# Kernel tuning notes

Measured on AMD Instinct MI355X. Metric: run time of the kernel, lower is better.

The kernel has to match this reference:

```python
import jax, jax.numpy as jnp
import numpy as np


def setup_inputs() -> dict:
    key = jax.random.key(0)
    k1, k2, k3 = jax.random.split(key, 3)
    B, H, S, D = 2, 16, 2048, 64
    q = jax.random.normal(k1, (B, H, S, D), dtype=jnp.float32)
    k = jax.random.normal(k2, (B, H, S, D), dtype=jnp.float32)
    v = jax.random.normal(k3, (B, H, S, D), dtype=jnp.float32)
    return {"q": q, "k": k, "v": v}


def reference(q, k, v):
    # q,k,v: [B,H,S,D]; causal attention with 1/sqrt(D) scaling, fp32 softmax.
    scale = 1.0 / (q.shape[-1] ** 0.5)
    scores = jnp.einsum('bhqd,bhkd->bhqk', q * scale, k)  # [B,H,S,S]
    S = scores.shape[-1]
    causal_mask = jnp.triu(jnp.ones((S, S), dtype=bool), k=1)
    scores = jnp.where(causal_mask, -jnp.inf, scores)
    attn = jax.nn.softmax(scores.astype(jnp.float32), axis=-1).astype(q.dtype)
    output = jnp.einsum('bhqk,bhkd->bhqd', attn, v)
    # Module also returns an all-zeros attn_weights placeholder of shape [B,H,S,S]
    attn_weights = jnp.zeros(scores.shape, dtype=q.dtype)
    return (output, attn_weights)
```

## Files before the change

### kernel.cpp

```cpp
#include <hip/hip_runtime.h>


typedef __bf16 bf16x8 __attribute__((ext_vector_type(8)));
typedef float f32x4 __attribute__((ext_vector_type(4)));

#define LOG2E 1.44269504088896340736f

__device__ __forceinline__ unsigned short f2bf(float f) {
  unsigned int u = __float_as_uint(f);
  u += 0x7fffu + ((u >> 16) & 1u);
  return (unsigned short)(u >> 16);
}

constexpr int Sdim = 2048, Ddim = 64, BHn = 32;
constexpr int STiles = 16;
constexpr int LDK = 72;
constexpr int OUT0 = BHn * Sdim * Ddim;
constexpr size_t FILL_PER_BH = 1048576;

__device__ __forceinline__ int vswz_m(int d) { return ((d >> 2) ^ (d >> 5)) & 7; }

__global__ __launch_bounds__(256, 2)
void flash_causal_kernel(const float* __restrict__ Q, const float* __restrict__ K,
                         const float* __restrict__ V, float* __restrict__ out) {
  __shared__ unsigned short Klds[2][64 * LDK];
  __shared__ unsigned short Vlds[2][64 * LDK];
  __shared__ unsigned short Plds[4][2][16 * LDK];

  const int tid  = threadIdx.x;
  const int wave = tid >> 6;
  const int lane = tid & 63;
  const int quad = lane >> 4;
  const int l15  = lane & 15;

  const int bh = blockIdx.x & (BHn - 1);
  const int g  = (int)(blockIdx.x >> 5);
  const int s  = (g & 1) ? (STiles - 1) - (g >> 1) : (g >> 1);
  const int jmax = 2 * s + 1;

  const int base  = bh * Sdim * Ddim;
  const int qbase = s * 128;

  bf16x8 aq[2][2];
  #pragma unroll
  for (int f = 0; f < 2; ++f) {
    const float* qp = Q + base + (qbase + 64 * f + wave * 16 + l15) * Ddim + quad * 8;
    #pragma unroll
    for (int s2 = 0; s2 < 2; ++s2) {
      float4 a = *(const float4*)(qp + 32 * s2);
      float4 b = *(const float4*)(qp + 32 * s2 + 4);
      union { unsigned short u[8]; bf16x8 v; } u;
      u.u[0] = f2bf(a.x * 0.125f); u.u[1] = f2bf(a.y * 0.125f);
      u.u[2] = f2bf(a.z * 0.125f); u.u[3] = f2bf(a.w * 0.125f);
      u.u[4] = f2bf(b.x * 0.125f); u.u[5] = f2bf(b.y * 0.125f);
      u.u[6] = f2bf(b.z * 0.125f); u.u[7] = f2bf(b.w * 0.125f);
      aq[f][s2] = u.v;
    }
  }

  f32x4 ot[2][4];
  #pragma unroll
  for (int f = 0; f < 2; ++f)
    #pragma unroll
    for (int t = 0; t < 4; ++t) ot[f][t] = (f32x4){0.f, 0.f, 0.f, 0.f};
  float mrun[2] = {-__builtin_inff(), -__builtin_inff()};
  float lrun[2] = {0.f, 0.f};

  const float4* kg4 = (const float4*)(K + base);
  const float4* vg4 = (const float4*)(V + base);
  float4 kf[4], vf[4];

  auto ldtile = [&](int j) {
    const float4* kp = kg4 + j * 1024;
    const float4* vp = vg4 + j * 1024;
    #pragma unroll
    for (int i = 0; i < 4; ++i) { kf[i] = kp[i * 256 + tid]; vf[i] = vp[i * 256 + tid]; }
  };
  auto stage = [&](int buf) {
    #pragma unroll
    for (int i = 0; i < 4; ++i) {
      int lin = i * 256 + tid;
      int row = lin >> 4;
      int c4  = (lin & 15) << 2;
      uint2 t2;
      t2.x = (unsigned int)f2bf(kf[i].x) | ((unsigned int)f2bf(kf[i].y) << 16);
      t2.y = (unsigned int)f2bf(kf[i].z) | ((unsigned int)f2bf(kf[i].w) << 16);
      *(uint2*)&Klds[buf][row * LDK + c4] = t2;
      const int sw = vswz_m(c4) << 3;
      Vlds[buf][(c4 + 0) * LDK + (row ^ sw)] = f2bf(vf[i].x);
      Vlds[buf][(c4 + 1) * LDK + (row ^ sw)] = f2bf(vf[i].y);
      Vlds[buf][(c4 + 2) * LDK + (row ^ sw)] = f2bf(vf[i].z);
      Vlds[buf][(c4 + 3) * LDK + (row ^ sw)] = f2bf(vf[i].w);
    }
  };

  ldtile(0); stage(0); ldtile(1);

  for (int j = 0; j <= jmax; ++j) {
    __syncthreads();
    if (j < jmax) stage((j + 1) & 1);
    if (j + 2 <= jmax) ldtile(j + 2);

    const unsigned short* Kb = Klds[j & 1];
    const unsigned short* Vb = Vlds[j & 1];
    const bool f0act = (j <= 2 * s);

    f32x4 sc[2][4];
    #pragma unroll
    for (int f = 0; f < 2; ++f)
      #pragma unroll
      for (int t = 0; t < 4; ++t) sc[f][t] = (f32x4){0.f, 0.f, 0.f, 0.f};
    #pragma unroll
    for (int s2 = 0; s2 < 2; ++s2) {
      #pragma unroll
      for (int t = 0; t < 4; ++t) {
        bf16x8 ka = *(const bf16x8*)&Kb[(16 * t + l15) * LDK + 32 * s2 + quad * 8];
        sc[0][t] = __builtin_amdgcn_mfma_f32_16x16x32_bf16(ka, aq[0][s2], sc[0][t], 0, 0, 0);
        sc[1][t] = __builtin_amdgcn_mfma_f32_16x16x32_bf16(ka, aq[1][s2], sc[1][t], 0, 0, 0);
      }
    }

    #pragma unroll
    for (int f = 0; f < 2; ++f) {
      if (j == 2 * s + f) {
        const int qml = wave * 16 + l15;
        #pragma unroll
        for (int t = 0; t < 4; ++t)
          #pragma unroll
          for (int r = 0; r < 4; ++r)
            if (16 * t + 4 * quad + r > qml) sc[f][t][r] = -__builtin_inff();
      }
    }

    #pragma unroll
    for (int f = 0; f < 2; ++f) {
      if (f == 0 && !f0act) continue;
      float mx = sc[f][0][0];
      #pragma unroll
      for (int t = 0; t < 4; ++t)
        #pragma unroll
        for (int r = 0; r < 4; ++r) mx = fmaxf(mx, sc[f][t][r]);
      mx = fmaxf(mx, __shfl_xor(mx, 16));
      mx = fmaxf(mx, __shfl_xor(mx, 32));
      float mn    = fmaxf(mrun[f], mx);
      float alpha = __builtin_amdgcn_exp2f((mrun[f] - mn) * LOG2E);
      float msc   = mn * LOG2E;
      mrun[f] = mn;
      float rs = 0.f;
      #pragma unroll
      for (int t = 0; t < 4; ++t)
        #pragma unroll
        for (int r = 0; r < 4; ++r) {
          float p = __builtin_amdgcn_exp2f(fmaf(sc[f][t][r], LOG2E, -msc));
          sc[f][t][r] = p;
          rs += p;
        }
      rs += __shfl_xor(rs, 16);
      rs += __shfl_xor(rs, 32);
      lrun[f] = lrun[f] * alpha + rs;
      #pragma unroll
      for (int t = 0; t < 4; ++t)
        #pragma unroll
        for (int r = 0; r < 4; ++r) ot[f][t][r] *= alpha;
      #pragma unroll
      for (int t = 0; t < 4; ++t) {
        uint2 pw;
        pw.x = (unsigned int)f2bf(sc[f][t][0]) | ((unsigned int)f2bf(sc[f][t][1]) << 16);
        pw.y = (unsigned int)f2bf(sc[f][t][2]) | ((unsigned int)f2bf(sc[f][t][3]) << 16);
        *(uint2*)&Plds[wave][f][l15 * LDK + 16 * t + 4 * quad] = pw;
      }
    }

    #pragma unroll
    for (int s2 = 0; s2 < 2; ++s2) {
      bf16x8 pb0, pb1;
      if (f0act) pb0 = *(const bf16x8*)&Plds[wave][0][l15 * LDK + 32 * s2 + quad * 8];
      pb1 = *(const bf16x8*)&Plds[wave][1][l15 * LDK + 32 * s2 + quad * 8];
      #pragma unroll
      for (int t = 0; t < 4; ++t) {
        const int d = 16 * t + l15;
        bf16x8 va = *(const bf16x8*)&Vb[d * LDK + (((4 * s2 + quad) ^ vswz_m(d)) << 3)];
        if (f0act)
          ot[0][t] = __builtin_amdgcn_mfma_f32_16x16x32_bf16(va, pb0, ot[0][t], 0, 0, 0);
        ot[1][t] = __builtin_amdgcn_mfma_f32_16x16x32_bf16(va, pb1, ot[1][t], 0, 0, 0);
      }
    }
  }

  #pragma unroll
  for (int f = 0; f < 2; ++f) {
    float inv = 1.0f / lrun[f];
    float* orow = out + base + (qbase + 64 * f + wave * 16 + l15) * Ddim + 4 * quad;
    #pragma unroll
    for (int t = 0; t < 4; ++t) {
      f32x4 o4;
      o4.x = ot[f][t][0] * inv; o4.y = ot[f][t][1] * inv;
      o4.z = ot[f][t][2] * inv; o4.w = ot[f][t][3] * inv;
      *(f32x4*)(orow + 16 * t) = o4;
    }
  }

  {
    const int gp = (STiles - 1) - s;
    const int w  = 2 * gp + 1;
    const size_t start_f4 = (size_t)bh * FILL_PER_BH + (size_t)4096 * (gp * gp);
    const size_t count_f4 = (size_t)4096 * w;
    f32x4 z4 = (f32x4){0.f, 0.f, 0.f, 0.f};
    f32x4* zp = (f32x4*)(out + OUT0) + start_f4;
    for (size_t i = tid; i < count_f4; i += 256)
      __builtin_nontemporal_store(z4, zp + i);
  }
}

extern "C" void kernel_launch(void* const* d_in, const int* in_sizes, int n_in,
                              void* d_out, int out_size, void* d_ws, size_t ws_size,
                              hipStream_t stream) {
  const float* q = (const float*)d_in[0];
  const float* k = (const float*)d_in[1];
  const float* v = (const float*)d_in[2];
  float* out = (float*)d_out;
  dim3 grid(BHn * STiles);
  flash_causal_kernel<<<grid, dim3(256), 0, stream>>>(q, k, v, out);
}
```

Baseline: 586.6 us.

## Read K/V directly from global memory in fp16, drop LDS staging

Removes the double-buffered LDS staging of K and V and its barriers. Each wave now loads fp32 K and V straight from global memory (V with strided scalar loads) and converts them to fp16 using packed round-toward-zero conversions. MFMA switches from bf16 to f16, block scheduling becomes plain sequential in place of interleaved heavy/light tiles, and the zero fill is split evenly per block with ordinary stores in place of nontemporal ones. In exchange, each wave re-reads K and V from memory or cache, and the V loads are uncoalesced, so memory traffic and load latency per tile go up.

```diff
diff --git a/kernel.cpp b/kernel.cpp
--- a/kernel.cpp
+++ b/kernel.cpp
@@ -1,31 +1,31 @@
 #include <hip/hip_runtime.h>
 
 
-typedef __bf16 bf16x8 __attribute__((ext_vector_type(8)));
+typedef __fp16 f16x2 __attribute__((ext_vector_type(2)));
+typedef __fp16 f16x4 __attribute__((ext_vector_type(4)));
+typedef __fp16 f16x8 __attribute__((ext_vector_type(8)));
 typedef float f32x4 __attribute__((ext_vector_type(4)));
 
 #define LOG2E 1.44269504088896340736f
-
-__device__ __forceinline__ unsigned short f2bf(float f) {
-  unsigned int u = __float_as_uint(f);
-  u += 0x7fffu + ((u >> 16) & 1u);
-  return (unsigned short)(u >> 16);
-}
 
 constexpr int Sdim = 2048, Ddim = 64, BHn = 32;
 constexpr int STiles = 16;
 constexpr int LDK = 72;
 constexpr int OUT0 = BHn * Sdim * Ddim;
-constexpr size_t FILL_PER_BH = 1048576;
 
-__device__ __forceinline__ int vswz_m(int d) { return ((d >> 2) ^ (d >> 5)) & 7; }
+__device__ __forceinline__ f16x8 cvt8(float4 a, float4 b) {
+  union { f16x2 h2[4]; f16x8 v; } u;
+  u.h2[0] = __builtin_amdgcn_cvt_pkrtz(a.x, a.y);
+  u.h2[1] = __builtin_amdgcn_cvt_pkrtz(a.z, a.w);
+  u.h2[2] = __builtin_amdgcn_cvt_pkrtz(b.x, b.y);
+  u.h2[3] = __builtin_amdgcn_cvt_pkrtz(b.z, b.w);
+  return u.v;
+}
 
 __global__ __launch_bounds__(256, 2)
 void flash_causal_kernel(const float* __restrict__ Q, const float* __restrict__ K,
                          const float* __restrict__ V, float* __restrict__ out) {
-  __shared__ unsigned short Klds[2][64 * LDK];
-  __shared__ unsigned short Vlds[2][64 * LDK];
-  __shared__ unsigned short Plds[4][2][16 * LDK];
+  __shared__ __fp16 Plds[4][2][16 * LDK];
 
   const int tid  = threadIdx.x;
   const int wave = tid >> 6;
@@ -34,27 +34,25 @@
   const int l15  = lane & 15;
 
   const int bh = blockIdx.x & (BHn - 1);
-  const int g  = (int)(blockIdx.x >> 5);
-  const int s  = (g & 1) ? (STiles - 1) - (g >> 1) : (g >> 1);
+  const int s  = (int)(blockIdx.x >> 5);
   const int jmax = 2 * s + 1;
 
   const int base  = bh * Sdim * Ddim;
   const int qbase = s * 128;
 
-  bf16x8 aq[2][2];
+  f16x8 aq[2][2];
   #pragma unroll
   for (int f = 0; f < 2; ++f) {
-    const float* qp = Q + base + (qbase + 64 * f + wave * 16 + l15) * Ddim + quad * 8;
     #pragma unroll
     for (int s2 = 0; s2 < 2; ++s2) {
-      float4 a = *(const float4*)(qp + 32 * s2);
-      float4 b = *(const float4*)(qp + 32 * s2 + 4);
-      union { unsigned short u[8]; bf16x8 v; } u;
-      u.u[0] = f2bf(a.x * 0.125f); u.u[1] = f2bf(a.y * 0.125f);
-      u.u[2] = f2bf(a.z * 0.125f); u.u[3] = f2bf(a.w * 0.125f);
-      u.u[4] = f2bf(b.x * 0.125f); u.u[5] = f2bf(b.y * 0.125f);
-      u.u[6] = f2bf(b.z * 0.125f); u.u[7] = f2bf(b.w * 0.125f);
-      aq[f][s2] = u.v;
+      const float* qp = Q + base + (qbase + 64 * f + wave * 16 + l15) * Ddim
+                          + 32 * s2 + 8 * quad;
+      float4 a = *(const float4*)qp;
+      float4 b = *(const float4*)(qp + 4);
+      float4 as, bs;
+      as.x = a.x * 0.125f; as.y = a.y * 0.125f; as.z = a.z * 0.125f; as.w = a.w * 0.125f;
+      bs.x = b.x * 0.125f; bs.y = b.y * 0.125f; bs.z = b.z * 0.125f; bs.w = b.w * 0.125f;
+      aq[f][s2] = cvt8(as, bs);
     }
   }
 
@@ -66,43 +64,9 @@
   float mrun[2] = {-__builtin_inff(), -__builtin_inff()};
   float lrun[2] = {0.f, 0.f};
 
-  const float4* kg4 = (const float4*)(K + base);
-  const float4* vg4 = (const float4*)(V + base);
-  float4 kf[4], vf[4];
-
-  auto ldtile = [&](int j) {
-    const float4* kp = kg4 + j * 1024;
-    const float4* vp = vg4 + j * 1024;
-    #pragma unroll
-    for (int i = 0; i < 4; ++i) { kf[i] = kp[i * 256 + tid]; vf[i] = vp[i * 256 + tid]; }
-  };
-  auto stage = [&](int buf) {
-    #pragma unroll
-    for (int i = 0; i < 4; ++i) {
-      int lin = i * 256 + tid;
-      int row = lin >> 4;
-      int c4  = (lin & 15) << 2;
-      uint2 t2;
-      t2.x = (unsigned int)f2bf(kf[i].x) | ((unsigned int)f2bf(kf[i].y) << 16);
-      t2.y = (unsigned int)f2bf(kf[i].z) | ((unsigned int)f2bf(kf[i].w) << 16);
-      *(uint2*)&Klds[buf][row * LDK + c4] = t2;
-      const int sw = vswz_m(c4) << 3;
-      Vlds[buf][(c4 + 0) * LDK + (row ^ sw)] = f2bf(vf[i].x);
-      Vlds[buf][(c4 + 1) * LDK + (row ^ sw)] = f2bf(vf[i].y);
-      Vlds[buf][(c4 + 2) * LDK + (row ^ sw)] = f2bf(vf[i].z);
-      Vlds[buf][(c4 + 3) * LDK + (row ^ sw)] = f2bf(vf[i].w);
-    }
-  };
-
-  ldtile(0); stage(0); ldtile(1);
-
   for (int j = 0; j <= jmax; ++j) {
-    __syncthreads();
-    if (j < jmax) stage((j + 1) & 1);
-    if (j + 2 <= jmax) ldtile(j + 2);
-
-    const unsigned short* Kb = Klds[j & 1];
-    const unsigned short* Vb = Vlds[j & 1];
+    const float* kb = K + base + (64 * j) * Ddim;
+    const float* vb = V + base + (64 * j) * Ddim;
     const bool f0act = (j <= 2 * s);
 
     f32x4 sc[2][4];
@@ -114,9 +78,12 @@
     for (int s2 = 0; s2 < 2; ++s2) {
       #pragma unroll
       for (int t = 0; t < 4; ++t) {
-        bf16x8 ka = *(const bf16x8*)&Kb[(16 * t + l15) * LDK + 32 * s2 + quad * 8];
-        sc[0][t] = __builtin_amdgcn_mfma_f32_16x16x32_bf16(ka, aq[0][s2], sc[0][t], 0, 0, 0);
-        sc[1][t] = __builtin_amdgcn_mfma_f32_16x16x32_bf16(ka, aq[1][s2], sc[1][t], 0, 0, 0);
+        const float* kp = kb + (16 * t + l15) * Ddim + 32 * s2 + 8 * quad;
+        float4 a = *(const float4*)kp;
+        float4 b = *(const float4*)(kp + 4);
+        f16x8 ka = cvt8(a, b);
+        sc[0][t] = __builtin_amdgcn_mfma_f32_16x16x32_f16(ka, aq[0][s2], sc[0][t], 0, 0, 0);
+        sc[1][t] = __builtin_amdgcn_mfma_f32_16x16x32_f16(ka, aq[1][s2], sc[1][t], 0, 0, 0);
       }
     }
 
@@ -164,25 +131,29 @@
         for (int r = 0; r < 4; ++r) ot[f][t][r] *= alpha;
       #pragma unroll
       for (int t = 0; t < 4; ++t) {
-        uint2 pw;
-        pw.x = (unsigned int)f2bf(sc[f][t][0]) | ((unsigned int)f2bf(sc[f][t][1]) << 16);
-        pw.y = (unsigned int)f2bf(sc[f][t][2]) | ((unsigned int)f2bf(sc[f][t][3]) << 16);
-        *(uint2*)&Plds[wave][f][l15 * LDK + 16 * t + 4 * quad] = pw;
+        union { f16x2 h2[2]; f16x4 v; } pu;
+        pu.h2[0] = __builtin_amdgcn_cvt_pkrtz(sc[f][t][0], sc[f][t][1]);
+        pu.h2[1] = __builtin_amdgcn_cvt_pkrtz(sc[f][t][2], sc[f][t][3]);
+        *(f16x4*)&Plds[wave][f][l15 * LDK + 16 * t + 4 * quad] = pu.v;
       }
     }
 
     #pragma unroll
     for (int s2 = 0; s2 < 2; ++s2) {
-      bf16x8 pb0, pb1;
-      if (f0act) pb0 = *(const bf16x8*)&Plds[wave][0][l15 * LDK + 32 * s2 + quad * 8];
-      pb1 = *(const bf16x8*)&Plds[wave][1][l15 * LDK + 32 * s2 + quad * 8];
+      f16x8 pb0, pb1;
+      if (f0act) pb0 = *(const f16x8*)&Plds[wave][0][l15 * LDK + 32 * s2 + 8 * quad];
+      pb1 = *(const f16x8*)&Plds[wave][1][l15 * LDK + 32 * s2 + 8 * quad];
+      const float* vp = vb + (32 * s2 + 8 * quad) * Ddim + l15;
       #pragma unroll
       for (int t = 0; t < 4; ++t) {
-        const int d = 16 * t + l15;
-        bf16x8 va = *(const bf16x8*)&Vb[d * LDK + (((4 * s2 + quad) ^ vswz_m(d)) << 3)];
+        float4 a, b;
+        const float* vt = vp + 16 * t;
+        a.x = vt[0];        a.y = vt[Ddim];     a.z = vt[2 * Ddim]; a.w = vt[3 * Ddim];
+        b.x = vt[4 * Ddim]; b.y = vt[5 * Ddim]; b.z = vt[6 * Ddim]; b.w = vt[7 * Ddim];
+        f16x8 va = cvt8(a, b);
         if (f0act)
-          ot[0][t] = __builtin_amdgcn_mfma_f32_16x16x32_bf16(va, pb0, ot[0][t], 0, 0, 0);
-        ot[1][t] = __builtin_amdgcn_mfma_f32_16x16x32_bf16(va, pb1, ot[1][t], 0, 0, 0);
+          ot[0][t] = __builtin_amdgcn_mfma_f32_16x16x32_f16(va, pb0, ot[0][t], 0, 0, 0);
+        ot[1][t] = __builtin_amdgcn_mfma_f32_16x16x32_f16(va, pb1, ot[1][t], 0, 0, 0);
       }
     }
   }
@@ -201,14 +172,11 @@
   }
 
   {
-    const int gp = (STiles - 1) - s;
-    const int w  = 2 * gp + 1;
-    const size_t start_f4 = (size_t)bh * FILL_PER_BH + (size_t)4096 * (gp * gp);
-    const size_t count_f4 = (size_t)4096 * w;
     f32x4 z4 = (f32x4){0.f, 0.f, 0.f, 0.f};
-    f32x4* zp = (f32x4*)(out + OUT0) + start_f4;
-    for (size_t i = tid; i < count_f4; i += 256)
-      __builtin_nontemporal_store(z4, zp + i);
+    f32x4* zp = (f32x4*)(out + OUT0) + (size_t)blockIdx.x * 65536 + tid;
+    #pragma unroll 8
+    for (int i = 0; i < 256; ++i)
+      zp[i * 256] = z4;
   }
 }
 
```

Result: slower. 747.0 us (+27.3%).
